# Kernel optimization log

Hardware: AMD Instinct MI355X
Metric: run time of the kernel (lower is better)

Reference implementation:

```python
import jax, jax.numpy as jnp
import numpy as np

D = 1024  # input_dim == output_dim
B = 4096  # batch (acts as sequence for batch-wise self-attention)


def setup_inputs() -> dict:
    key = jax.random.key(0)
    k1, k2, k3, k4 = jax.random.split(key, 4)
    inputs = jax.random.normal(k1, (B, D), dtype=jnp.float32)
    rotation_params = jax.random.normal(k2, (D, D), dtype=jnp.float32)
    # torch nn.Linear(input_dim, output_dim): weight (out, in), bias (out,)
    linear_w = jax.random.normal(k3, (D, D), dtype=jnp.float32) * (1.0 / np.sqrt(D))
    linear_b = jax.random.normal(k4, (D,), dtype=jnp.float32) * 0.01
    return {"inputs": inputs, "rotation_params": rotation_params,
            "linear_w": linear_w, "linear_b": linear_b}


def reference(inputs, rotation_params, linear_w, linear_b):
    # query = X R ; key = X R^T  -> scores = softmax(Q K^T / sqrt(D)) over batch dim
    query = inputs @ rotation_params                 # [B, D]
    key = inputs @ rotation_params.T                 # [B, D]
    scale = 1.0 / np.sqrt(D).astype(np.float32)
    scores = jax.nn.softmax(jnp.einsum('bd,cd->bc', query, key) * scale, axis=-1)  # [B, B]
    weighted = scores @ inputs                        # [B, D]
    return weighted @ linear_w.T + linear_b           # [B, out]
```

## Files before the change

kernel.cpp:

```cpp
#include <hip/hip_runtime.h>
#include <math.h>
#include <stdint.h>

using f16 = _Float16;
using half8 = __attribute__((ext_vector_type(8))) f16;
using half4 = __attribute__((ext_vector_type(4))) f16;
using f32x4 = __attribute__((ext_vector_type(4))) float;

__device__ __forceinline__ void gl_lds16(const f16* g, f16* l) {
  __builtin_amdgcn_global_load_lds(
      (const __attribute__((address_space(1))) void*)g,
      (__attribute__((address_space(3))) void*)l, 16, 0, 0);
}

__global__ __launch_bounds__(512, 2) void gemm_q2(
    const f16* __restrict__ Ap, const f16* __restrict__ Bp,
    float* __restrict__ C, int N, int K, long sAp, long sBp, float scale) {
  __shared__ f16 lds[2 * 4096 * 8];
  const int tid = threadIdx.x;
  const int lane = tid & 63;
  const int wave = tid >> 6;
  const int wr = (wave >> 2) * 128;
  const int wc = (wave & 3) * 64;

  const int nwg = gridDim.x * gridDim.y;
  int bid = blockIdx.y * gridDim.x + blockIdx.x;
  bid = (bid & 7) * (nwg >> 3) + (bid >> 3);
  const int bm = (bid / gridDim.x) * 256;
  const int bn = (bid % gridDim.x) * 256;

  const int nt = K / 32;

  auto stage = [&](int t, int i) {
    const int g0 = i * 512 + wave * 64;
    const int ga = g0 + lane;
    const bool isB = ga >= 2048;
    const int gl = ga & 2047;
    const int pl = gl >> 10;
    const int gp = gl & 1023;
    const int r = gp >> 2;
    const int cg = (gp & 3) ^ ((r >> 1) & 3);
    const f16* gs = (isB ? Bp + (size_t)pl * sBp + (size_t)(bn + r) * K
                         : Ap + (size_t)pl * sAp + (size_t)(bm + r) * K) +
                    t * 32 + cg * 8;
    gl_lds16(gs, &lds[((size_t)(t & 1) * 4096 + g0) * 8]);
  };

  int aoff[2][8], boff[2][4];
#pragma unroll
  for (int pl = 0; pl < 2; ++pl) {
#pragma unroll
    for (int fr = 0; fr < 8; ++fr) {
      const int row = wr + fr * 16 + (lane & 15);
      const int kg = (lane >> 4) ^ ((row >> 1) & 3);
      aoff[pl][fr] = (pl * 1024 + row * 4 + kg) * 8;
    }
#pragma unroll
    for (int fc = 0; fc < 4; ++fc) {
      const int col = wc + fc * 16 + (lane & 15);
      const int kg = (lane >> 4) ^ ((col >> 1) & 3);
      boff[pl][fc] = (2048 + pl * 1024 + col * 4 + kg) * 8;
    }
  }

  f32x4 acc[8][4];
#pragma unroll
  for (int m = 0; m < 8; ++m)
#pragma unroll
    for (int n = 0; n < 4; ++n) acc[m][n] = (f32x4){0.f, 0.f, 0.f, 0.f};

  half8 af[2][4], bf[2][2];

#define LOAD_A(h)                                            \
  _Pragma("unroll") for (int pl = 0; pl < 2; ++pl)           \
      _Pragma("unroll") for (int i = 0; i < 4; ++i) af[pl][i] = \
          *(const half8*)&buf[aoff[pl][(h) * 4 + i]];
#define LOAD_B(h)                                            \
  _Pragma("unroll") for (int pl = 0; pl < 2; ++pl)           \
      _Pragma("unroll") for (int j = 0; j < 2; ++j) bf[pl][j] = \
          *(const half8*)&buf[boff[pl][(h) * 2 + j]];
#define MFMA_Q(ah, bh)                                                        \
  _Pragma("unroll") for (int i = 0; i < 4; ++i) _Pragma("unroll") for (int j = \
                                                                          0;  \
                                                                       j < 2; \
                                                                       ++j) { \
    acc[(ah) * 4 + i][(bh) * 2 + j] = __builtin_amdgcn_mfma_f32_16x16x32_f16( \
        af[0][i], bf[0][j], acc[(ah) * 4 + i][(bh) * 2 + j], 0, 0, 0);        \
    acc[(ah) * 4 + i][(bh) * 2 + j] = __builtin_amdgcn_mfma_f32_16x16x32_f16( \
        af[0][i], bf[1][j], acc[(ah) * 4 + i][(bh) * 2 + j], 0, 0, 0);        \
    acc[(ah) * 4 + i][(bh) * 2 + j] = __builtin_amdgcn_mfma_f32_16x16x32_f16( \
        af[1][i], bf[0][j], acc[(ah) * 4 + i][(bh) * 2 + j], 0, 0, 0);        \
  }
#define PHASE_TAIL()                                    \
  __builtin_amdgcn_sched_barrier(0);                    \
  asm volatile("s_barrier" ::: "memory");               \
  asm volatile("s_waitcnt lgkmcnt(0)" ::: "memory");    \
  __builtin_amdgcn_sched_barrier(0);                    \
  __builtin_amdgcn_s_setprio(1);
#define PHASE_END()                                     \
  __builtin_amdgcn_s_setprio(0);                        \
  __builtin_amdgcn_sched_barrier(0);                    \
  asm volatile("s_barrier" ::: "memory");

#pragma unroll
  for (int i = 0; i < 8; ++i) stage(0, i);

  for (int t = 0; t < nt; ++t) {
    const f16* buf = &lds[(size_t)(t & 1) * 4096 * 8];
    asm volatile("s_waitcnt vmcnt(0)" ::: "memory");
    asm volatile("s_barrier" ::: "memory");
    const bool pf = (t + 1 < nt);

    LOAD_A(0);
    LOAD_B(0);
    if (pf) { stage(t + 1, 0); stage(t + 1, 1); stage(t + 1, 2); }
    PHASE_TAIL();
    MFMA_Q(0, 0);
    PHASE_END();

    LOAD_B(1);
    if (pf) { stage(t + 1, 3); stage(t + 1, 4); stage(t + 1, 5); }
    PHASE_TAIL();
    MFMA_Q(0, 1);
    PHASE_END();

    LOAD_A(1);
    if (pf) { stage(t + 1, 6); stage(t + 1, 7); }
    PHASE_TAIL();
    MFMA_Q(1, 1);
    PHASE_END();

    LOAD_B(0);
    PHASE_TAIL();
    MFMA_Q(1, 0);
    __builtin_amdgcn_s_setprio(0);
    __builtin_amdgcn_sched_barrier(0);
  }
#undef LOAD_A
#undef LOAD_B
#undef MFMA_Q
#undef PHASE_TAIL
#undef PHASE_END

#pragma unroll
  for (int m = 0; m < 8; ++m) {
#pragma unroll
    for (int n = 0; n < 4; ++n) {
      const int col = bn + wc + n * 16 + (lane & 15);
#pragma unroll
      for (int q = 0; q < 4; ++q) {
        const int row = bm + wr + m * 16 + (lane >> 4) * 4 + q;
        C[(size_t)row * N + col] = acc[m][n][q] * scale;
      }
    }
  }
}

template <int NP, int EPI, bool BIASF>
__global__ __launch_bounds__(512, 2) void gemm_dp(
    const f16* __restrict__ Ap, const f16* __restrict__ Bp,
    void* __restrict__ Cv, const float* __restrict__ bias, int M, int N, int K,
    long sAp, long sBp, long sCp, float scale) {
  __shared__ f16 lds[3 * 2048 * 8];
  const int tid = threadIdx.x;
  const int lane = tid & 63;
  const int wave = tid >> 6;
  const int wr = (wave >> 1) * 32;
  const int wc = (wave & 1) * 64;

  const int nwg = gridDim.x * gridDim.y;
  int bid = blockIdx.y * gridDim.x + blockIdx.x;
  bid = (bid & 7) * (nwg >> 3) + (bid >> 3);
  const int bm = (bid / gridDim.x) * 128;
  const int bn = (bid % gridDim.x) * 128;

  constexpr int KSTEP = (NP == 2) ? 32 : 64;
  const int nt = K / KSTEP;

  auto stage = [&](int t, int i) {
    const int g0 = i * 512 + wave * 64;
    const int ga = g0 + lane;
    const bool isB = ga >= 1024;
    const int gl = ga & 1023;
    const int pl = gl >> 9;
    const int gp = gl & 511;
    const int r = gp >> 2;
    const int cg = (gp & 3) ^ ((r >> 1) & 3);
    const long sP = (NP == 2) ? (isB ? sBp : sAp) : 0;
    const int kOff = (NP == 2) ? 0 : pl * 32;
    const f16* gs = (isB ? Bp : Ap) + (size_t)pl * sP +
                    (size_t)((isB ? bn : bm) + r) * K + t * KSTEP + kOff +
                    cg * 8;
    gl_lds16(gs, &lds[((size_t)(t % 3) * 2048 + g0) * 8]);
  };

  int aoff[2][2], boff[2][4];
#pragma unroll
  for (int pl = 0; pl < 2; ++pl) {
#pragma unroll
    for (int m = 0; m < 2; ++m) {
      const int row = wr + m * 16 + (lane & 15);
      const int kg = (lane >> 4) ^ ((row >> 1) & 3);
      aoff[pl][m] = (pl * 512 + row * 4 + kg) * 8;
    }
#pragma unroll
    for (int n = 0; n < 4; ++n) {
      const int col = wc + n * 16 + (lane & 15);
      const int kg = (lane >> 4) ^ ((col >> 1) & 3);
      boff[pl][n] = (1024 + pl * 512 + col * 4 + kg) * 8;
    }
  }

  f32x4 acc[2][4];
#pragma unroll
  for (int m = 0; m < 2; ++m)
#pragma unroll
    for (int n = 0; n < 4; ++n) acc[m][n] = (f32x4){0.f, 0.f, 0.f, 0.f};

#pragma unroll
  for (int i = 0; i < 4; ++i) stage(0, i);
#pragma unroll
  for (int i = 0; i < 4; ++i) stage(1, i);

  for (int t = 0; t < nt; ++t) {
    const f16* buf = &lds[(size_t)(t % 3) * 2048 * 8];
    if (t + 1 < nt)
      asm volatile("s_waitcnt vmcnt(4)" ::: "memory");
    else
      asm volatile("s_waitcnt vmcnt(0)" ::: "memory");
    asm volatile("s_barrier" ::: "memory");

    half8 af[2][2], b0[2][2];
#pragma unroll
    for (int pl = 0; pl < 2; ++pl) {
#pragma unroll
      for (int m = 0; m < 2; ++m) af[pl][m] = *(const half8*)&buf[aoff[pl][m]];
#pragma unroll
      for (int j = 0; j < 2; ++j) b0[pl][j] = *(const half8*)&buf[boff[pl][j]];
    }
    if (t + 2 < nt) {
      stage(t + 2, 0);
      stage(t + 2, 1);
    }
    __builtin_amdgcn_sched_barrier(0);
    asm volatile("s_barrier" ::: "memory");
    asm volatile("s_waitcnt lgkmcnt(0)" ::: "memory");
    __builtin_amdgcn_sched_barrier(0);
    __builtin_amdgcn_s_setprio(1);
#pragma unroll
    for (int m = 0; m < 2; ++m) {
#pragma unroll
      for (int j = 0; j < 2; ++j) {
        acc[m][j] = __builtin_amdgcn_mfma_f32_16x16x32_f16(af[0][m], b0[0][j],
                                                           acc[m][j], 0, 0, 0);
        if (NP == 2) {
          acc[m][j] = __builtin_amdgcn_mfma_f32_16x16x32_f16(
              af[0][m], b0[1][j], acc[m][j], 0, 0, 0);
          acc[m][j] = __builtin_amdgcn_mfma_f32_16x16x32_f16(
              af[1][m], b0[0][j], acc[m][j], 0, 0, 0);
        } else {
          acc[m][j] = __builtin_amdgcn_mfma_f32_16x16x32_f16(
              af[1][m], b0[1][j], acc[m][j], 0, 0, 0);
        }
      }
    }
    __builtin_amdgcn_s_setprio(0);
    __builtin_amdgcn_sched_barrier(0);
    asm volatile("s_barrier" ::: "memory");

    half8 b1[2][2];
#pragma unroll
    for (int pl = 0; pl < 2; ++pl)
#pragma unroll
      for (int j = 0; j < 2; ++j)
        b1[pl][j] = *(const half8*)&buf[boff[pl][2 + j]];
    if (t + 2 < nt) {
      stage(t + 2, 2);
      stage(t + 2, 3);
    }
    __builtin_amdgcn_sched_barrier(0);
    asm volatile("s_barrier" ::: "memory");
    asm volatile("s_waitcnt lgkmcnt(0)" ::: "memory");
    __builtin_amdgcn_sched_barrier(0);
    __builtin_amdgcn_s_setprio(1);
#pragma unroll
    for (int m = 0; m < 2; ++m) {
#pragma unroll
      for (int j = 0; j < 2; ++j) {
        acc[m][2 + j] = __builtin_amdgcn_mfma_f32_16x16x32_f16(
            af[0][m], b1[0][j], acc[m][2 + j], 0, 0, 0);
        if (NP == 2) {
          acc[m][2 + j] = __builtin_amdgcn_mfma_f32_16x16x32_f16(
              af[0][m], b1[1][j], acc[m][2 + j], 0, 0, 0);
          acc[m][2 + j] = __builtin_amdgcn_mfma_f32_16x16x32_f16(
              af[1][m], b1[0][j], acc[m][2 + j], 0, 0, 0);
        } else {
          acc[m][2 + j] = __builtin_amdgcn_mfma_f32_16x16x32_f16(
              af[1][m], b1[1][j], acc[m][2 + j], 0, 0, 0);
        }
      }
    }
    __builtin_amdgcn_s_setprio(0);
    __builtin_amdgcn_sched_barrier(0);
  }

#pragma unroll
  for (int m = 0; m < 2; ++m) {
#pragma unroll
    for (int n = 0; n < 4; ++n) {
      const int col = bn + wc + n * 16 + (lane & 15);
      const float bv = BIASF ? bias[col] : 0.f;
#pragma unroll
      for (int q = 0; q < 4; ++q) {
        const int row = bm + wr + m * 16 + (lane >> 4) * 4 + q;
        float v = acc[m][n][q] * scale;
        if (EPI == 0) {
          ((float*)Cv)[(size_t)row * N + col] = v + bv;
        } else if (EPI == 1) {
          f16* C = (f16*)Cv;
          const f16 h = (f16)v;
          C[(size_t)row * N + col] = h;
          C[sCp + (size_t)row * N + col] = (f16)(v - (float)h);
        } else {
          ((f16*)Cv)[(size_t)row * N + col] = (f16)v;
        }
      }
    }
  }
}

template <int NP, int TN, int EPI, bool BIASF, int MINW>
__global__ __launch_bounds__(256, MINW) void gemm_mp(
    const f16* __restrict__ Ap, const f16* __restrict__ Bp,
    void* __restrict__ Cv, const float* __restrict__ bias, int M, int N, int K,
    long sAp, long sBp, long sCp, float scale) {
  constexpr int FR = (TN == 128) ? 4 : 2;
  constexpr int FC = 4;
  constexpr int AG = NP * 512;
  constexpr int BPG = TN * 4;
  __shared__ f16 As[NP * 128 * 32];
  __shared__ f16 Bs[NP * TN * 32];
  const int tid = threadIdx.x;
  const int lane = tid & 63;
  const int wave = tid >> 6;
  const int wr = (TN == 128) ? (wave >> 1) * 64 : wave * 32;
  const int wc = (TN == 128) ? (wave & 1) * 64 : 0;

  const int nwg = gridDim.x * gridDim.y;
  int bid = blockIdx.y * gridDim.x + blockIdx.x;
  bid = (bid & 7) * (nwg >> 3) + (bid >> 3);
  const int bm = (bid / gridDim.x) * 128;
  const int bn = (bid % gridDim.x) * TN;

  int aoff[NP][FR], boff[NP][FC];
#pragma unroll
  for (int p = 0; p < NP; ++p) {
#pragma unroll
    for (int m = 0; m < FR; ++m) {
      const int row = wr + m * 16 + (lane & 15);
      const int kga = (lane >> 4) ^ ((row >> 1) & 3);
      aoff[p][m] = (p * 512 + row * 4 + kga) * 8;
    }
#pragma unroll
    for (int n = 0; n < FC; ++n) {
      const int col = wc + n * 16 + (lane & 15);
      const int kgb = (lane >> 4) ^ ((col >> 1) & 3);
      boff[p][n] = (p * BPG + col * 4 + kgb) * 8;
    }
  }

  f32x4 acc[FR][FC];
#pragma unroll
  for (int m = 0; m < FR; ++m)
#pragma unroll
    for (int n = 0; n < FC; ++n) acc[m][n] = (f32x4){0.f, 0.f, 0.f, 0.f};

  for (int k0 = 0; k0 < K; k0 += 32) {
#pragma unroll
    for (int i = 0; i < (NP * (512 + TN * 4)) / 256; ++i) {
      const int g0 = i * 256 + wave * 64;
      const bool isB = g0 >= AG;
      const int ga0 = g0 - (isB ? AG : 0);
      const int ga = ga0 + lane;
      const int pl = isB ? (ga / BPG) : (ga >> 9);
      const int gp = isB ? (ga % BPG) : (ga & 511);
      const int r = gp >> 2;
      const int cg = (gp & 3) ^ ((r >> 1) & 3);
      const f16* gs = (isB ? Bp + (size_t)pl * sBp + (size_t)(bn + r) * K
                           : Ap + (size_t)pl * sAp + (size_t)(bm + r) * K) +
                      k0 + cg * 8;
      f16* ld = (isB ? Bs : As) + (size_t)ga0 * 8;
      gl_lds16(gs, ld);
    }
    __syncthreads();

    half8 af[NP][FR], bf[NP][FC];
#pragma unroll
    for (int p = 0; p < NP; ++p) {
#pragma unroll
      for (int m = 0; m < FR; ++m) af[p][m] = *(const half8*)&As[aoff[p][m]];
#pragma unroll
      for (int n = 0; n < FC; ++n) bf[p][n] = *(const half8*)&Bs[boff[p][n]];
    }
#pragma unroll
    for (int m = 0; m < FR; ++m) {
#pragma unroll
      for (int n = 0; n < FC; ++n) {
        acc[m][n] = __builtin_amdgcn_mfma_f32_16x16x32_f16(af[0][m], bf[0][n],
                                                           acc[m][n], 0, 0, 0);
        if (NP == 2) {
          acc[m][n] = __builtin_amdgcn_mfma_f32_16x16x32_f16(
              af[0][m], bf[1][n], acc[m][n], 0, 0, 0);
          acc[m][n] = __builtin_amdgcn_mfma_f32_16x16x32_f16(
              af[1][m], bf[0][n], acc[m][n], 0, 0, 0);
        }
      }
    }
    __syncthreads();
  }

#pragma unroll
  for (int m = 0; m < FR; ++m) {
#pragma unroll
    for (int n = 0; n < FC; ++n) {
      const int col = bn + wc + n * 16 + (lane & 15);
      const float bv = BIASF ? bias[col] : 0.f;
#pragma unroll
      for (int q = 0; q < 4; ++q) {
        const int row = bm + wr + m * 16 + (lane >> 4) * 4 + q;
        float v = acc[m][n][q] * scale;
        if (EPI == 0) {
          ((float*)Cv)[(size_t)row * N + col] = v + bv;
        } else if (EPI == 1) {
          f16* C = (f16*)Cv;
          const f16 h = (f16)v;
          C[(size_t)row * N + col] = h;
          C[sCp + (size_t)row * N + col] = (f16)(v - (float)h);
        } else {
          ((f16*)Cv)[(size_t)row * N + col] = (f16)v;
        }
      }
    }
  }
}

template <int NP>
__global__ __launch_bounds__(256) void split_n(const float* __restrict__ in,
                                               f16* __restrict__ out,
                                               long planeStride, int n4) {
  const int i = blockIdx.x * 256 + threadIdx.x;
  if (i >= n4) return;
  const float4 v = ((const float4*)in)[i];
  const float vv[4] = {v.x, v.y, v.z, v.w};
  half4 h, mm;
#pragma unroll
  for (int q = 0; q < 4; ++q) {
    h[q] = (f16)vv[q];
    if (NP == 2) mm[q] = (f16)(vv[q] - (float)h[q]);
  }
  ((half4*)out)[i] = h;
  if (NP == 2) ((half4*)(out + planeStride))[i] = mm;
}

template <int NP>
__global__ __launch_bounds__(256) void split_t(const float* __restrict__ in,
                                               f16* __restrict__ out, int Mr,
                                               int Nc, long planeStride) {
  __shared__ float Ls[64][65];
  const int i0 = blockIdx.y * 64;
  const int j0 = blockIdx.x * 64;
  const int t = threadIdx.x;
  const int r = t >> 4;
  const int c = (t & 15) * 4;
#pragma unroll
  for (int i = 0; i < 4; ++i) {
    const float4 v =
        *(const float4*)&in[(size_t)(i0 + r + i * 16) * Nc + j0 + c];
    Ls[r + i * 16][c + 0] = v.x;
    Ls[r + i * 16][c + 1] = v.y;
    Ls[r + i * 16][c + 2] = v.z;
    Ls[r + i * 16][c + 3] = v.w;
  }
  __syncthreads();
#pragma unroll
  for (int i = 0; i < 4; ++i) {
    const int r2 = r + i * 16;
    half4 h, mm;
#pragma unroll
    for (int q = 0; q < 4; ++q) {
      const float v = Ls[c + q][r2];
      h[q] = (f16)v;
      if (NP == 2) mm[q] = (f16)(v - (float)h[q]);
    }
    *(half4*)&out[(size_t)(j0 + r2) * Mr + i0 + c] = h;
    if (NP == 2)
      *(half4*)&out[planeStride + (size_t)(j0 + r2) * Mr + i0 + c] = mm;
  }
}

__global__ __launch_bounds__(256) void softmax_p16(const float* __restrict__ L,
                                                   f16* __restrict__ P) {
  const int row = blockIdx.x;
  const float* p = L + (size_t)row * 4096;
  f16* o = P + (size_t)row * 4096;
  const int tid = threadIdx.x;
  __shared__ float red[8];

  float m = -INFINITY;
  for (int i = tid * 4; i < 4096; i += 1024) {
    const float4 v = *reinterpret_cast<const float4*>(&p[i]);
    m = fmaxf(fmaxf(fmaxf(v.x, v.y), fmaxf(v.z, v.w)), m);
  }
#pragma unroll
  for (int off = 32; off > 0; off >>= 1) m = fmaxf(m, __shfl_xor(m, off));
  if ((tid & 63) == 0) red[tid >> 6] = m;
  __syncthreads();
  m = fmaxf(fmaxf(red[0], red[1]), fmaxf(red[2], red[3]));

  float s = 0.f;
  for (int i = tid * 4; i < 4096; i += 1024) {
    const float4 v = *reinterpret_cast<const float4*>(&p[i]);
    s += expf(v.x - m) + expf(v.y - m) + expf(v.z - m) + expf(v.w - m);
  }
#pragma unroll
  for (int off = 32; off > 0; off >>= 1) s += __shfl_xor(s, off);
  if ((tid & 63) == 0) red[4 + (tid >> 6)] = s;
  __syncthreads();
  s = red[4] + red[5] + red[6] + red[7];
  const float inv = 1.0f / s;

  for (int i = tid * 4; i < 4096; i += 1024) {
    const float4 v = *reinterpret_cast<const float4*>(&p[i]);
    half4 h;
    h[0] = (f16)(expf(v.x - m) * inv);
    h[1] = (f16)(expf(v.y - m) * inv);
    h[2] = (f16)(expf(v.z - m) * inv);
    h[3] = (f16)(expf(v.w - m) * inv);
    *(half4*)&o[i] = h;
  }
}

extern "C" void kernel_launch(void* const* d_in, const int* in_sizes, int n_in,
                              void* d_out, int out_size, void* d_ws,
                              size_t ws_size, hipStream_t stream) {
  const float* X = (const float*)d_in[0];
  const float* R = (const float*)d_in[1];
  const float* Wl = (const float*)d_in[2];
  const float* bias = (const float*)d_in[3];
  float* out = (float*)d_out;

  const int Bq = 4096, D = 1024;
  const size_t MiB = 1 << 20;
  uint8_t* w8 = (uint8_t*)d_ws;
  f16* Xp = (f16*)(w8);
  f16* Tp = (f16*)(w8 + 16 * MiB);
  f16* Pp = (f16*)(w8);
  f16* Wp = (f16*)(w8 + 32 * MiB);
  f16* Rp = (f16*)(w8 + 36 * MiB);
  f16* Rtp = (f16*)(w8 + 40 * MiB);
  f16* Mtp = (f16*)(w8 + 44 * MiB);
  float* L = (float*)(w8 + 36 * MiB);
  f16* Xh = (f16*)(w8 + 36 * MiB);
  f16* Yt = (f16*)(w8 + 44 * MiB);

  const long sR = (long)D * D, sX = (long)Bq * D;
  const dim3 blk(256), blk512(512);

  split_n<2><<<D * D / 1024, blk, 0, stream>>>(R, Rp, sR, D * D / 4);
  split_t<2><<<dim3(D / 64, D / 64), blk, 0, stream>>>(R, Rtp, D, D, sR);
  split_n<2><<<Bq * D / 1024, blk, 0, stream>>>(X, Xp, sX, Bq * D / 4);
  split_n<1><<<D * D / 1024, blk, 0, stream>>>(Wl, Wp, 0, D * D / 4);

  gemm_mp<2, 64, 1, false, 2><<<dim3(D / 64, D / 128), blk, 0, stream>>>(
      Rtp, Rp, Mtp, nullptr, D, D, D, sR, sR, sR, 1.f);
  gemm_dp<2, 1, false><<<dim3(D / 128, Bq / 128), blk512, 0, stream>>>(
      Xp, Mtp, Tp, nullptr, Bq, D, D, sX, sR, sX, 1.f);
  gemm_q2<<<dim3(Bq / 256, Bq / 256), blk512, 0, stream>>>(
      Tp, Xp, L, Bq, D, sX, sX, 0.03125f);
  softmax_p16<<<dim3(Bq), blk, 0, stream>>>(L, Pp);
  split_n<1><<<Bq * D / 1024, blk, 0, stream>>>(X, Xh, 0, Bq * D / 4);
  gemm_dp<1, 2, false><<<dim3(Bq / 128, D / 128), blk512, 0, stream>>>(
      Wp, Xh, Yt, nullptr, D, Bq, D, 0, 0, 0, 1.f);
  gemm_dp<1, 0, true><<<dim3(D / 128, Bq / 128), blk512, 0, stream>>>(
      Pp, Yt, out, bias, Bq, D, Bq, 0, 0, 0, 1.f);
}
```

Baseline: 259.2 us.

## Double-buffer register fragments in gemm_q2 and cache softmax row in LDS

The gemm_q2 main loop now double-buffers the A/B fragment registers and drops the per-phase s_barrier and lgkmcnt waits. This lets LDS reads for the next quarter overlap with MFMAs on the current one, and the global-to-LDS prefetch stages are regrouped into two batches of four. Separately, the softmax kernel caches each row in shared memory and stores the exponentials there. That removes two extra global reads and one redundant expf pass. The trade-offs are higher register pressure in the GEMM, reliance on the compiler to insert the right waits once the explicit barriers are gone, and 16KB of LDS per softmax block.

```diff
diff --git a/kernel.cpp b/kernel.cpp
--- a/kernel.cpp
+++ b/kernel.cpp
@@ -69,38 +69,25 @@
 #pragma unroll
     for (int n = 0; n < 4; ++n) acc[m][n] = (f32x4){0.f, 0.f, 0.f, 0.f};
 
-  half8 af[2][4], bf[2][2];
-
-#define LOAD_A(h)                                            \
-  _Pragma("unroll") for (int pl = 0; pl < 2; ++pl)           \
-      _Pragma("unroll") for (int i = 0; i < 4; ++i) af[pl][i] = \
+  half8 af0[2][4], af1[2][4], bf0[2][2], bf1[2][2];
+
+#define LOAD_A(dst, h)                                          \
+  _Pragma("unroll") for (int pl = 0; pl < 2; ++pl)              \
+      _Pragma("unroll") for (int i = 0; i < 4; ++i) dst[pl][i] = \
           *(const half8*)&buf[aoff[pl][(h) * 4 + i]];
-#define LOAD_B(h)                                            \
-  _Pragma("unroll") for (int pl = 0; pl < 2; ++pl)           \
-      _Pragma("unroll") for (int j = 0; j < 2; ++j) bf[pl][j] = \
+#define LOAD_B(dst, h)                                          \
+  _Pragma("unroll") for (int pl = 0; pl < 2; ++pl)              \
+      _Pragma("unroll") for (int j = 0; j < 2; ++j) dst[pl][j] = \
           *(const half8*)&buf[boff[pl][(h) * 2 + j]];
-#define MFMA_Q(ah, bh)                                                        \
-  _Pragma("unroll") for (int i = 0; i < 4; ++i) _Pragma("unroll") for (int j = \
-                                                                          0;  \
-                                                                       j < 2; \
-                                                                       ++j) { \
-    acc[(ah) * 4 + i][(bh) * 2 + j] = __builtin_amdgcn_mfma_f32_16x16x32_f16( \
-        af[0][i], bf[0][j], acc[(ah) * 4 + i][(bh) * 2 + j], 0, 0, 0);        \
-    acc[(ah) * 4 + i][(bh) * 2 + j] = __builtin_amdgcn_mfma_f32_16x16x32_f16( \
-        af[0][i], bf[1][j], acc[(ah) * 4 + i][(bh) * 2 + j], 0, 0, 0);        \
-    acc[(ah) * 4 + i][(bh) * 2 + j] = __builtin_amdgcn_mfma_f32_16x16x32_f16( \
-        af[1][i], bf[0][j], acc[(ah) * 4 + i][(bh) * 2 + j], 0, 0, 0);        \
-  }
-#define PHASE_TAIL()                                    \
-  __builtin_amdgcn_sched_barrier(0);                    \
-  asm volatile("s_barrier" ::: "memory");               \
-  asm volatile("s_waitcnt lgkmcnt(0)" ::: "memory");    \
-  __builtin_amdgcn_sched_barrier(0);                    \
-  __builtin_amdgcn_s_setprio(1);
-#define PHASE_END()                                     \
-  __builtin_amdgcn_s_setprio(0);                        \
-  __builtin_amdgcn_sched_barrier(0);                    \
-  asm volatile("s_barrier" ::: "memory");
+#define MFMA_Q(A, B, ah, bh)                                                  \
+  _Pragma("unroll") for (int i = 0; i < 4; ++i)                               \
+      _Pragma("unroll") for (int j = 0; j < 2; ++j) {                         \
+    f32x4& c = acc[(ah) * 4 + i][(bh) * 2 + j];                               \
+    c = __builtin_amdgcn_mfma_f32_16x16x32_f16(A[0][i], B[0][j], c, 0, 0, 0); \
+    c = __builtin_amdgcn_mfma_f32_16x16x32_f16(A[0][i], B[1][j], c, 0, 0, 0); \
+    c = __builtin_amdgcn_mfma_f32_16x16x32_f16(A[1][i], B[0][j], c, 0, 0, 0); \
+  }
+#define SBAR0() __builtin_amdgcn_sched_barrier(0)
 
 #pragma unroll
   for (int i = 0; i < 8; ++i) stage(0, i);
@@ -111,36 +98,38 @@
     asm volatile("s_barrier" ::: "memory");
     const bool pf = (t + 1 < nt);
 
-    LOAD_A(0);
-    LOAD_B(0);
-    if (pf) { stage(t + 1, 0); stage(t + 1, 1); stage(t + 1, 2); }
-    PHASE_TAIL();
-    MFMA_Q(0, 0);
-    PHASE_END();
-
-    LOAD_B(1);
-    if (pf) { stage(t + 1, 3); stage(t + 1, 4); stage(t + 1, 5); }
-    PHASE_TAIL();
-    MFMA_Q(0, 1);
-    PHASE_END();
-
-    LOAD_A(1);
-    if (pf) { stage(t + 1, 6); stage(t + 1, 7); }
-    PHASE_TAIL();
-    MFMA_Q(1, 1);
-    PHASE_END();
-
-    LOAD_B(0);
-    PHASE_TAIL();
-    MFMA_Q(1, 0);
+    LOAD_A(af0, 0);
+    LOAD_B(bf0, 0);
+    if (pf) { stage(t + 1, 0); stage(t + 1, 1); stage(t + 1, 2); stage(t + 1, 3); }
+    SBAR0();
+    LOAD_B(bf1, 1);
+    SBAR0();
+    __builtin_amdgcn_s_setprio(1);
+    MFMA_Q(af0, bf0, 0, 0);
     __builtin_amdgcn_s_setprio(0);
-    __builtin_amdgcn_sched_barrier(0);
+    SBAR0();
+    LOAD_A(af1, 1);
+    if (pf) { stage(t + 1, 4); stage(t + 1, 5); stage(t + 1, 6); stage(t + 1, 7); }
+    SBAR0();
+    __builtin_amdgcn_s_setprio(1);
+    MFMA_Q(af0, bf1, 0, 1);
+    __builtin_amdgcn_s_setprio(0);
+    SBAR0();
+    LOAD_B(bf0, 0);
+    SBAR0();
+    __builtin_amdgcn_s_setprio(1);
+    MFMA_Q(af1, bf1, 1, 1);
+    __builtin_amdgcn_s_setprio(0);
+    SBAR0();
+    __builtin_amdgcn_s_setprio(1);
+    MFMA_Q(af1, bf0, 1, 0);
+    __builtin_amdgcn_s_setprio(0);
+    SBAR0();
   }
 #undef LOAD_A
 #undef LOAD_B
 #undef MFMA_Q
-#undef PHASE_TAIL
-#undef PHASE_END
+#undef SBAR0
 
 #pragma unroll
   for (int m = 0; m < 8; ++m) {
@@ -500,15 +489,17 @@
 
 __global__ __launch_bounds__(256) void softmax_p16(const float* __restrict__ L,
                                                    f16* __restrict__ P) {
-  const int row = blockIdx.x;
-  const float* p = L + (size_t)row * 4096;
-  f16* o = P + (size_t)row * 4096;
+  __shared__ float row[4096];
+  __shared__ float red[8];
+  const int rix = blockIdx.x;
+  const float* p = L + (size_t)rix * 4096;
+  f16* o = P + (size_t)rix * 4096;
   const int tid = threadIdx.x;
-  __shared__ float red[8];
 
   float m = -INFINITY;
   for (int i = tid * 4; i < 4096; i += 1024) {
     const float4 v = *reinterpret_cast<const float4*>(&p[i]);
+    *reinterpret_cast<float4*>(&row[i]) = v;
     m = fmaxf(fmaxf(fmaxf(v.x, v.y), fmaxf(v.z, v.w)), m);
   }
 #pragma unroll
@@ -519,8 +510,13 @@
 
   float s = 0.f;
   for (int i = tid * 4; i < 4096; i += 1024) {
-    const float4 v = *reinterpret_cast<const float4*>(&p[i]);
-    s += expf(v.x - m) + expf(v.y - m) + expf(v.z - m) + expf(v.w - m);
+    float4 v = *reinterpret_cast<const float4*>(&row[i]);
+    v.x = expf(v.x - m);
+    v.y = expf(v.y - m);
+    v.z = expf(v.z - m);
+    v.w = expf(v.w - m);
+    s += v.x + v.y + v.z + v.w;
+    *reinterpret_cast<float4*>(&row[i]) = v;
   }
 #pragma unroll
   for (int off = 32; off > 0; off >>= 1) s += __shfl_xor(s, off);
@@ -530,12 +526,12 @@
   const float inv = 1.0f / s;
 
   for (int i = tid * 4; i < 4096; i += 1024) {
-    const float4 v = *reinterpret_cast<const float4*>(&p[i]);
+    const float4 v = *reinterpret_cast<const float4*>(&row[i]);
     half4 h;
-    h[0] = (f16)(expf(v.x - m) * inv);
-    h[1] = (f16)(expf(v.y - m) * inv);
-    h[2] = (f16)(expf(v.z - m) * inv);
-    h[3] = (f16)(expf(v.w - m) * inv);
+    h[0] = (f16)(v.x * inv);
+    h[1] = (f16)(v.y * inv);
+    h[2] = (f16)(v.z * inv);
+    h[3] = (f16)(v.w * inv);
     *(half4*)&o[i] = h;
   }
 }
```

Result: faster. 246.1 us (-5.0%).
